# Optimization experiments

Hardware: AMD Instinct MI355X
Metric: run time of the kernel (lower is better)

Reference implementation:

```python
import jax, jax.numpy as jnp
import numpy as np
from jax import ops as jops

N_NODES = 100000
N_EDGES = 1600000
NEG_SLOPE = 0.2
LN_EPS = 1e-5


def setup_inputs() -> dict:
    key = jax.random.key(0)
    ks = jax.random.split(key, 12)
    inp = {
        "x": jax.random.normal(ks[0], (N_NODES, 4), jnp.float32),
        "edge_index": jax.random.randint(ks[1], (2, N_EDGES), 0, N_NODES, jnp.int64 if jax.config.jax_enable_x64 else jnp.int32),
        # layer 1: GATv2Conv(4, 16, heads=4)
        "W1l": jax.random.normal(ks[2], (4, 64), jnp.float32) * 0.5,
        "W1r": jax.random.normal(ks[3], (4, 64), jnp.float32) * 0.5,
        "a1": jax.random.normal(ks[4], (4, 16), jnp.float32) * 0.5,  # [heads, out]
        "b1": jax.random.normal(ks[5], (64,), jnp.float32) * 0.1,
        "g1": jnp.ones((64,), jnp.float32),
        "be1": jnp.zeros((64,), jnp.float32),
        # layer 2: GATv2Conv(64, 32, heads=1)
        "W2l": jax.random.normal(ks[6], (64, 32), jnp.float32) * 0.125,
        "W2r": jax.random.normal(ks[7], (64, 32), jnp.float32) * 0.125,
        "a2": jax.random.normal(ks[8], (1, 32), jnp.float32) * 0.5,
        "b2": jax.random.normal(ks[9], (32,), jnp.float32) * 0.1,
        "g2": jnp.ones((32,), jnp.float32),
        "be2": jnp.zeros((32,), jnp.float32),
    }
    return inp


def _add_self_loops(edge_index, n):
    loop = jnp.arange(n, dtype=edge_index.dtype)
    return jnp.concatenate([edge_index, jnp.stack([loop, loop])], axis=1)


def _gatv2(x, src, dst, Wl, Wr, att, bias, heads, out_ch, n):
    # x: [N, F]; Wl/Wr: [F, heads*out_ch]; att: [heads, out_ch]
    xl = (x @ Wl).reshape(n, heads, out_ch)  # source transform
    xr = (x @ Wr).reshape(n, heads, out_ch)  # target transform
    e = xl[src] + xr[dst]                     # [E, H, C]
    e = jnp.where(e >= 0, e, NEG_SLOPE * e)   # LeakyReLU(0.2)
    logits = jnp.einsum('ehc,hc->eh', e, att)  # [E, H]
    # segment softmax over destination node
    m = jops.segment_max(logits, dst, num_segments=n)  # [N, H]
    ex = jnp.exp(logits - m[dst])
    denom = jops.segment_sum(ex, dst, num_segments=n)  # [N, H]
    alpha = ex / denom[dst]                            # [E, H]
    out = jops.segment_sum(alpha[:, :, None] * xl[src], dst, num_segments=n)  # [N, H, C]
    return out.reshape(n, heads * out_ch) + bias


def _layernorm(x, g, b):
    mu = jnp.mean(x, axis=-1, keepdims=True)
    var = jnp.mean(jnp.square(x - mu), axis=-1, keepdims=True)
    return (x - mu) * jax.lax.rsqrt(var + LN_EPS) * g + b


def reference(x, edge_index, W1l, W1r, a1, b1, g1, be1, W2l, W2r, a2, b2, g2, be2):
    n = x.shape[0]
    ei = _add_self_loops(edge_index, n)
    src, dst = ei[0], ei[1]
    h = _gatv2(x, src, dst, W1l, W1r, a1, b1, heads=4, out_ch=16, n=n)
    h = _layernorm(h, g1, be1)
    h = jnp.where(h > 0, h, jnp.expm1(h))  # ELU
    h = _gatv2(h, src, dst, W2l, W2r, a2, b2, heads=1, out_ch=32, n=n)
    h = _layernorm(h, g2, be2)
    return h
```

## Files before the change

### kernel.cpp

```cpp
#include <hip/hip_runtime.h>
#include <math.h>

#define NN 100000
#define E0 1600000
#define ETOT (E0 + NN)
#define NEG 0.2f

#define NB 512
#define BS 196
#define CHUNK 4096
#define PPT 16
#define MAXP 4096

template <int CTRL>
__device__ __forceinline__ float dppadd(float v) {
    int t = __builtin_amdgcn_update_dpp(0, __float_as_int(v), CTRL, 0xf, 0xf, true);
    return v + __int_as_float(t);
}
__device__ __forceinline__ float wsum64(float v) {
    v = dppadd<0xB1>(v);
    v = dppadd<0x4E>(v);
    v = dppadd<0x141>(v);
    v = dppadd<0x140>(v);
    v += __shfl_xor(v, 16);
    v += __shfl_xor(v, 32);
    return v;
}
__device__ __forceinline__ unsigned f2bf_rn(float f) {
    unsigned u = __float_as_uint(f);
    return (u + 0x7FFFu + ((u >> 16) & 1u)) >> 16;
}

__global__ void k_bhist(const int* __restrict__ ei, int* __restrict__ bcnt) {
    __shared__ int h[NB];
    int tid = threadIdx.x;
    for (int i = tid; i < NB; i += 256) h[i] = 0;
    __syncthreads();
    int stride = gridDim.x * 256;
    for (int e = blockIdx.x * 256 + tid; e < E0; e += stride)
        atomicAdd(&h[ei[E0 + e] / BS], 1);
    __syncthreads();
    for (int i = tid; i < NB; i += 256)
        if (h[i]) atomicAdd(&bcnt[i], h[i]);
}

__global__ void k_bscan(const int* __restrict__ bcnt, int* __restrict__ boff,
                        int* __restrict__ srcsBase, int* __restrict__ cursor,
                        int* __restrict__ rs) {
    __shared__ int s[NB];
    int tid = threadIdx.x;
    int v = bcnt[tid];
    s[tid] = v;
    __syncthreads();
    for (int off = 1; off < NB; off <<= 1) {
        int t = (tid >= off) ? s[tid - off] : 0;
        __syncthreads();
        s[tid] += t;
        __syncthreads();
    }
    int excl = s[tid] - v;
    boff[tid] = excl;
    cursor[tid] = excl;
    int n0 = tid * BS;
    if (n0 > NN) n0 = NN;
    srcsBase[tid] = excl + n0;
    if (tid == 0) rs[NN] = ETOT;
}

__global__ void k_bin(const int* __restrict__ ei, int* __restrict__ cursor,
                      int2* __restrict__ binned) {
    __shared__ int hist[NB];
    __shared__ int basesh[NB];
    int tid = threadIdx.x;
    long long cbase = (long long)blockIdx.x * CHUNK;
    for (int i = tid; i < NB; i += 256) hist[i] = 0;
    __syncthreads();
    int srcv[PPT], dstv[PPT], rank[PPT], bkt[PPT];
#pragma unroll
    for (int k = 0; k < PPT; ++k) {
        long long e = cbase + k * 256 + tid;
        if (e < E0) {
            int s_ = ei[e];
            int d_ = ei[E0 + e];
            int b = d_ / BS;
            rank[k] = atomicAdd(&hist[b], 1);
            srcv[k] = s_;
            dstv[k] = d_;
            bkt[k] = b;
        } else {
            bkt[k] = -1;
        }
    }
    __syncthreads();
    for (int i = tid; i < NB; i += 256)
        if (hist[i] > 0) basesh[i] = atomicAdd(&cursor[i], hist[i]);
    __syncthreads();
#pragma unroll
    for (int k = 0; k < PPT; ++k)
        if (bkt[k] >= 0) {
            int2 p;
            p.x = srcv[k];
            p.y = dstv[k];
            binned[basesh[bkt[k]] + rank[k]] = p;
        }
}

__global__ void k_bfin(const int2* __restrict__ binned, const int* __restrict__ bcnt,
                       const int* __restrict__ boff, const int* __restrict__ srcsBase,
                       int* __restrict__ rs, int* __restrict__ srcs) {
    int b = blockIdx.x;
    int n0 = b * BS;
    if (n0 >= NN) return;
    int nd = NN - n0;
    if (nd > BS) nd = BS;
    int cnt = bcnt[b];
    if (cnt > MAXP) cnt = MAXP;
    int base = boff[b];
    int sb = srcsBase[b];
    __shared__ int ldsCnt[256];
    __shared__ int scanA[256];
    __shared__ int rowOffE[256];
    __shared__ int stage[MAXP + BS];
    int tid = threadIdx.x;
    ldsCnt[tid] = 0;
    __syncthreads();
    int srcv[PPT], dl_[PPT], rk_[PPT];
#pragma unroll
    for (int k = 0; k < PPT; ++k) {
        int i = k * 256 + tid;
        if (i < cnt) {
            int2 p = binned[base + i];
            int dl = p.y - n0;
            rk_[k] = atomicAdd(&ldsCnt[dl], 1);
            srcv[k] = p.x;
            dl_[k] = dl;
        } else {
            dl_[k] = -1;
        }
    }
    __syncthreads();
    int v = (tid < nd) ? ldsCnt[tid] + 1 : 0;
    scanA[tid] = v;
    __syncthreads();
    for (int off = 1; off < 256; off <<= 1) {
        int t = (tid >= off) ? scanA[tid - off] : 0;
        __syncthreads();
        scanA[tid] += t;
        __syncthreads();
    }
    rowOffE[tid] = scanA[tid] - v;
    __syncthreads();
    if (tid < nd) {
        int e = rowOffE[tid];
        rs[n0 + tid] = sb + e;
        stage[e] = n0 + tid;
    }
    __syncthreads();
#pragma unroll
    for (int k = 0; k < PPT; ++k)
        if (dl_[k] >= 0) stage[rowOffE[dl_[k]] + 1 + rk_[k]] = srcv[k];
    __syncthreads();
    int tot = cnt + nd;
    for (int i = tid; i < tot; i += 256) srcs[sb + i] = stage[i];
}

__global__ void k_linr(const float* __restrict__ x, const float* __restrict__ Wr,
                       float* __restrict__ xr1) {
    int t = blockIdx.x * blockDim.x + threadIdx.x;
    if (t >= NN * 16) return;
    int n = t >> 4;
    int j = (t & 15) << 2;
    const float4 xv = *(const float4*)(x + (long long)n * 4);
    float4 a = {0.f, 0.f, 0.f, 0.f};
#pragma unroll
    for (int k = 0; k < 4; ++k) {
        float4 w = *(const float4*)(Wr + k * 64 + j);
        float xk = k == 0 ? xv.x : k == 1 ? xv.y : k == 2 ? xv.z : xv.w;
        a.x += xk * w.x; a.y += xk * w.y;
        a.z += xk * w.z; a.w += xk * w.w;
    }
    *(float4*)(xr1 + (long long)n * 64 + j) = a;
}

__global__ __launch_bounds__(256, 5) void k_gat1(
        const float* __restrict__ x, const float* __restrict__ Wl,
        const float* __restrict__ xr1, const float* __restrict__ att,
        const int* __restrict__ rs, const int* __restrict__ srcs,
        const float* __restrict__ b, const float* __restrict__ g,
        const float* __restrict__ be, float* __restrict__ h) {
    int lane = threadIdx.x & 63;
    int wave = (blockIdx.x * blockDim.x + threadIdx.x) >> 6;
    int nwaves = (gridDim.x * blockDim.x) >> 6;
    int e_i = lane >> 3;
    int sub = lane & 7;
    float wl[4][8], at[8];
#pragma unroll
    for (int k = 0; k < 4; ++k)
#pragma unroll
        for (int j = 0; j < 8; ++j) wl[k][j] = Wl[k * 64 + sub * 8 + j];
#pragma unroll
    for (int j = 0; j < 8; ++j) at[j] = att[sub * 8 + j];

    for (int n = wave; n < NN; n += nwaves) {
        const float4 r0 = *(const float4*)(xr1 + (long long)n * 64 + sub * 8);
        const float4 r1 = *(const float4*)(xr1 + (long long)n * 64 + sub * 8 + 4);
        float xrd[8] = {r0.x, r0.y, r0.z, r0.w, r1.x, r1.y, r1.z, r1.w};
        int beg = rs[n];
        int end = rs[n + 1];
        float acc4[4] = {0.f, 0.f, 0.f, 0.f};
        float den = 0.f;
        int slot = beg + e_i;
        bool valid = slot < end;
        int s = srcs[valid ? slot : beg];
        float4 xa = *(const float4*)(x + (long long)s * 4);
        for (int base = beg; base < end; base += 8) {
            int nslot = base + 8 + e_i;
            bool nvalid = nslot < end;
            int ns = srcs[nvalid ? nslot : beg];
            float4 xn = *(const float4*)(x + (long long)ns * 4);
            float p = 0.f;
#pragma unroll
            for (int j = 0; j < 8; ++j) {
                float t = xa.x * wl[0][j] + xa.y * wl[1][j] + xa.z * wl[2][j] +
                          xa.w * wl[3][j];
                float u = t + xrd[j];
                u = fmaxf(u, NEG * u);
                p += u * at[j];
            }
            p = dppadd<0xB1>(p);
            float ex = valid ? __expf(p) : 0.f;
            den += ex;
            acc4[0] += ex * xa.x;
            acc4[1] += ex * xa.y;
            acc4[2] += ex * xa.z;
            acc4[3] += ex * xa.w;
            xa = xn;
            valid = nvalid;
        }
#pragma unroll
        for (int m = 8; m <= 32; m <<= 1) {
#pragma unroll
            for (int k = 0; k < 4; ++k) acc4[k] += __shfl_xor(acc4[k], m);
            den += __shfl_xor(den, m);
        }
        int cf = sub * 8 + e_i;
        float v = (acc4[0] * Wl[cf] + acc4[1] * Wl[64 + cf] +
                   acc4[2] * Wl[128 + cf] + acc4[3] * Wl[192 + cf]) / den + b[cf];
        float s1 = wsum64(v);
        float s2 = wsum64(v * v);
        float mu = s1 * (1.f / 64.f);
        float var = fmaxf(s2 * (1.f / 64.f) - mu * mu, 0.f);
        float y = (v - mu) * rsqrtf(var + 1e-5f) * g[cf] + be[cf];
        h[(long long)n * 64 + cf] = y > 0.f ? y : expm1f(y);
    }
}

__global__ void k_lin2(const float* __restrict__ h, const float* __restrict__ Wl,
                       const float* __restrict__ Wr, unsigned* __restrict__ xl2p,
                       float* __restrict__ xr2) {
    __shared__ float wl_s[2048];
    __shared__ float wr_s[2048];
    for (int i = threadIdx.x; i < 2048; i += blockDim.x) {
        wl_s[i] = Wl[i];
        wr_s[i] = Wr[i];
    }
    __syncthreads();
    int t = blockIdx.x * blockDim.x + threadIdx.x;
    if (t >= NN * 16) return;
    int n = t >> 4, j2 = t & 15;
    const float* hr = h + (long long)n * 64;
    float al0 = 0.f, al1 = 0.f, ar0 = 0.f, ar1 = 0.f;
#pragma unroll 8
    for (int k = 0; k < 64; ++k) {
        float hv = hr[k];
        al0 += hv * wl_s[k * 32 + j2 * 2];
        al1 += hv * wl_s[k * 32 + j2 * 2 + 1];
        ar0 += hv * wr_s[k * 32 + j2 * 2];
        ar1 += hv * wr_s[k * 32 + j2 * 2 + 1];
    }
    xl2p[(long long)n * 16 + j2] = (f2bf_rn(al1) << 16) | f2bf_rn(al0);
    *(float2*)(xr2 + (long long)n * 32 + j2 * 2) = {ar0, ar1};
}

__global__ void k_gat2(const unsigned* __restrict__ xl2p,
                       const float* __restrict__ xr2,
                       const float* __restrict__ att, const int* __restrict__ rs,
                       const int* __restrict__ srcs, const float* __restrict__ b,
                       const float* __restrict__ g, const float* __restrict__ be,
                       float* __restrict__ out) {
    int lane = threadIdx.x & 63;
    int wave = (blockIdx.x * blockDim.x + threadIdx.x) >> 6;
    int nwaves = (gridDim.x * blockDim.x) >> 6;
    int e_i = lane >> 3;
    int cg = lane & 7;
    float at[4];
#pragma unroll
    for (int j = 0; j < 4; ++j) at[j] = att[cg * 4 + j];

    for (int n = wave; n < NN; n += nwaves) {
        const float4 xr4 = *(const float4*)(xr2 + (long long)n * 32 + cg * 4);
        float xrd[4] = {xr4.x, xr4.y, xr4.z, xr4.w};
        int beg = rs[n];
        int end = rs[n + 1];
        float acc[4] = {0.f, 0.f, 0.f, 0.f};
        float den = 0.f;
        int slot = beg + e_i;
        bool valid = slot < end;
        int s = srcs[valid ? slot : beg];
        uint2 xp = *(const uint2*)(xl2p + (long long)s * 16 + cg * 2);
        for (int base = beg; base < end; base += 8) {
            int nslot = base + 8 + e_i;
            bool nvalid = nslot < end;
            int ns = srcs[nvalid ? nslot : beg];
            uint2 xq = *(const uint2*)(xl2p + (long long)ns * 16 + cg * 2);
            float xv0 = __uint_as_float(xp.x << 16);
            float xv1 = __uint_as_float(xp.x & 0xFFFF0000u);
            float xv2 = __uint_as_float(xp.y << 16);
            float xv3 = __uint_as_float(xp.y & 0xFFFF0000u);
            float u0 = xv0 + xrd[0], u1 = xv1 + xrd[1];
            float u2 = xv2 + xrd[2], u3 = xv3 + xrd[3];
            u0 = fmaxf(u0, NEG * u0);
            u1 = fmaxf(u1, NEG * u1);
            u2 = fmaxf(u2, NEG * u2);
            u3 = fmaxf(u3, NEG * u3);
            float p = u0 * at[0] + u1 * at[1] + u2 * at[2] + u3 * at[3];
            p = dppadd<0xB1>(p);
            p = dppadd<0x4E>(p);
            p = dppadd<0x141>(p);
            float ex = valid ? __expf(p) : 0.f;
            den += ex;
            acc[0] += ex * xv0;
            acc[1] += ex * xv1;
            acc[2] += ex * xv2;
            acc[3] += ex * xv3;
            xp = xq;
            valid = nvalid;
        }
#pragma unroll
        for (int m = 8; m <= 32; m <<= 1) {
#pragma unroll
            for (int j = 0; j < 4; ++j) acc[j] += __shfl_xor(acc[j], m);
            den += __shfl_xor(den, m);
        }
        int e3 = e_i & 3;
        float v = acc[0];
#pragma unroll
        for (int j = 1; j < 4; ++j) v = (e3 == j) ? acc[j] : v;
        int cf = cg * 4 + e3;
        v = v / den + b[cf];
        float mu = wsum64(v) * (1.f / 64.f);
        float cc = v - mu;
        float var = wsum64(cc * cc) * (1.f / 64.f);
        float y = cc * rsqrtf(var + 1e-5f) * g[cf] + be[cf];
        if (e_i < 4) out[(long long)n * 32 + cf] = y;
    }
}

extern "C" void kernel_launch(void* const* d_in, const int* in_sizes, int n_in,
                              void* d_out, int out_size, void* d_ws, size_t ws_size,
                              hipStream_t stream) {
    const float* x   = (const float*)d_in[0];
    const int*   ei  = (const int*)d_in[1];
    const float* W1l = (const float*)d_in[2];
    const float* W1r = (const float*)d_in[3];
    const float* a1  = (const float*)d_in[4];
    const float* b1  = (const float*)d_in[5];
    const float* g1  = (const float*)d_in[6];
    const float* be1 = (const float*)d_in[7];
    const float* W2l = (const float*)d_in[8];
    const float* W2r = (const float*)d_in[9];
    const float* a2  = (const float*)d_in[10];
    const float* b2  = (const float*)d_in[11];
    const float* g2  = (const float*)d_in[12];
    const float* be2 = (const float*)d_in[13];
    float* out = (float*)d_out;

    float* ws = (float*)d_ws;
    float* h   = ws;
    float* xr1 = ws + 6400000;
    unsigned* xl2p = (unsigned*)(ws + 6400000);
    float* xr2 = ws + 9600000;
    int2* binned = (int2*)ws;
    int* ib        = (int*)(ws + 12800000);
    int* rs        = ib;
    int* srcs      = ib + 100001;
    int* bcnt      = ib + 1800100;
    int* boff      = ib + 1800100 + NB;
    int* srcsBase  = ib + 1800100 + 2 * NB;
    int* cursor    = ib + 1800100 + 3 * NB;

    hipMemsetAsync(bcnt, 0, NB * sizeof(int), stream);
    k_bhist<<<256, 256, 0, stream>>>(ei, bcnt);
    k_bscan<<<1, NB, 0, stream>>>(bcnt, boff, srcsBase, cursor, rs);
    k_bin<<<(E0 + CHUNK - 1) / CHUNK, 256, 0, stream>>>(ei, cursor, binned);
    k_bfin<<<NB, 256, 0, stream>>>(binned, bcnt, boff, srcsBase, rs, srcs);
    k_linr<<<(NN * 16 + 255) / 256, 256, 0, stream>>>(x, W1r, xr1);

    k_gat1<<<2048, 256, 0, stream>>>(x, W1l, xr1, a1, rs, srcs, b1, g1, be1, h);
    k_lin2<<<(NN * 16 + 255) / 256, 256, 0, stream>>>(h, W2l, W2r, xl2p, xr2);
    k_gat2<<<2048, 256, 0, stream>>>(xl2p, xr2, a2, rs, srcs, b2, g2, be2, out);
}
```

Before: 221.5 us.

## Stage binned edges in LDS for coalesced writes; tune gat2 bounds and LN stats

The binning kernel now builds a per-block histogram, scans it, and reserves each bucket's global range up front. It then scatters the edges into an LDS staging buffer in bucket order and writes them out contiguously, so global stores are coalesced rather than scattered. This costs a second read of the edge indices, an extra LDS pass and more shared memory per block (about 32KB for staging), which may lower occupancy. Separately, k_gat2 gets launch bounds (256, 6), and its layernorm computes the sum and sum of squares as two independent reductions, which is less numerically stable.

```diff
diff --git a/kernel.cpp b/kernel.cpp
--- a/kernel.cpp
+++ b/kernel.cpp
@@ -70,39 +70,51 @@
 __global__ void k_bin(const int* __restrict__ ei, int* __restrict__ cursor,
                       int2* __restrict__ binned) {
     __shared__ int hist[NB];
-    __shared__ int basesh[NB];
+    __shared__ int loff[NB];
+    __shared__ int sbase[NB];
+    __shared__ int scanA[256];
+    __shared__ int2 stage[CHUNK];
     int tid = threadIdx.x;
-    long long cbase = (long long)blockIdx.x * CHUNK;
+    int e0 = blockIdx.x * CHUNK;
+    int ecnt = min(CHUNK, E0 - e0);
     for (int i = tid; i < NB; i += 256) hist[i] = 0;
     __syncthreads();
-    int srcv[PPT], dstv[PPT], rank[PPT], bkt[PPT];
-#pragma unroll
-    for (int k = 0; k < PPT; ++k) {
-        long long e = cbase + k * 256 + tid;
-        if (e < E0) {
-            int s_ = ei[e];
-            int d_ = ei[E0 + e];
-            int b = d_ / BS;
-            rank[k] = atomicAdd(&hist[b], 1);
-            srcv[k] = s_;
-            dstv[k] = d_;
-            bkt[k] = b;
-        } else {
-            bkt[k] = -1;
-        }
-    }
-    __syncthreads();
-    for (int i = tid; i < NB; i += 256)
-        if (hist[i] > 0) basesh[i] = atomicAdd(&cursor[i], hist[i]);
-    __syncthreads();
-#pragma unroll
-    for (int k = 0; k < PPT; ++k)
-        if (bkt[k] >= 0) {
-            int2 p;
-            p.x = srcv[k];
-            p.y = dstv[k];
-            binned[basesh[bkt[k]] + rank[k]] = p;
-        }
+    for (int i = tid; i < ecnt; i += 256)
+        atomicAdd(&hist[ei[E0 + e0 + i] / BS], 1);
+    __syncthreads();
+    int a = hist[2 * tid], b2 = hist[2 * tid + 1];
+    int tsum = a + b2;
+    scanA[tid] = tsum;
+    __syncthreads();
+    for (int off = 1; off < 256; off <<= 1) {
+        int t = (tid >= off) ? scanA[tid - off] : 0;
+        __syncthreads();
+        scanA[tid] += t;
+        __syncthreads();
+    }
+    int excl = scanA[tid] - tsum;
+    loff[2 * tid] = excl;
+    loff[2 * tid + 1] = excl + a;
+    if (a) sbase[2 * tid] = atomicAdd(&cursor[2 * tid], a);
+    if (b2) sbase[2 * tid + 1] = atomicAdd(&cursor[2 * tid + 1], b2);
+    __syncthreads();
+    for (int i = tid; i < NB; i += 256) hist[i] = loff[i];
+    __syncthreads();
+    for (int i = tid; i < ecnt; i += 256) {
+        int s_ = ei[e0 + i];
+        int d_ = ei[E0 + e0 + i];
+        int pos = atomicAdd(&hist[d_ / BS], 1);
+        int2 p;
+        p.x = s_;
+        p.y = d_;
+        stage[pos] = p;
+    }
+    __syncthreads();
+    for (int i = tid; i < ecnt; i += 256) {
+        int2 p = stage[i];
+        int b = p.y / BS;
+        binned[sbase[b] + (i - loff[b])] = p;
+    }
 }
 
 __global__ void k_bfin(const int2* __restrict__ binned, const int* __restrict__ bcnt,
@@ -282,12 +294,12 @@
     *(float2*)(xr2 + (long long)n * 32 + j2 * 2) = {ar0, ar1};
 }
 
-__global__ void k_gat2(const unsigned* __restrict__ xl2p,
-                       const float* __restrict__ xr2,
-                       const float* __restrict__ att, const int* __restrict__ rs,
-                       const int* __restrict__ srcs, const float* __restrict__ b,
-                       const float* __restrict__ g, const float* __restrict__ be,
-                       float* __restrict__ out) {
+__global__ __launch_bounds__(256, 6) void k_gat2(
+        const unsigned* __restrict__ xl2p, const float* __restrict__ xr2,
+        const float* __restrict__ att, const int* __restrict__ rs,
+        const int* __restrict__ srcs, const float* __restrict__ b,
+        const float* __restrict__ g, const float* __restrict__ be,
+        float* __restrict__ out) {
     int lane = threadIdx.x & 63;
     int wave = (blockIdx.x * blockDim.x + threadIdx.x) >> 6;
     int nwaves = (gridDim.x * blockDim.x) >> 6;
@@ -348,10 +360,11 @@
         for (int j = 1; j < 4; ++j) v = (e3 == j) ? acc[j] : v;
         int cf = cg * 4 + e3;
         v = v / den + b[cf];
-        float mu = wsum64(v) * (1.f / 64.f);
-        float cc = v - mu;
-        float var = wsum64(cc * cc) * (1.f / 64.f);
-        float y = cc * rsqrtf(var + 1e-5f) * g[cf] + be[cf];
+        float s1 = wsum64(v);
+        float s2 = wsum64(v * v);
+        float mu = s1 * (1.f / 64.f);
+        float var = fmaxf(s2 * (1.f / 64.f) - mu * mu, 0.f);
+        float y = (v - mu) * rsqrtf(var + 1e-5f) * g[cf] + be[cf];
         if (e_i < 4) out[(long long)n * 32 + cf] = y;
     }
 }
```

Result: slower. 230.3 us (+4.0%).
